# Kernel optimization log

Hardware: AMD Instinct MI355X
Metric: run time of the kernel (lower is better)

## Reference

```python
import jax, jax.numpy as jnp
import numpy as np

B, D, K, BETA = 32, 64, 1024, 0.25


def _conv(x, w, b, s=1, p=0):
    y = jax.lax.conv_general_dilated(x, w, (s, s), [(p, p), (p, p)],
                                     dimension_numbers=('NCHW', 'OIHW', 'NCHW'))
    return y + b[None, :, None, None]


def _tconv(x, w, b):
    # PyTorch ConvTranspose2d(k=4, s=2, p=1); w layout (C_in, C_out, 4, 4)
    wt = jnp.flip(w, (2, 3)).transpose(1, 0, 2, 3)
    y = jax.lax.conv_general_dilated(x, wt, (1, 1), [(2, 2), (2, 2)],
                                     lhs_dilation=(2, 2),
                                     dimension_numbers=('NCHW', 'OIHW', 'NCHW'))
    return y + b[None, :, None, None]


def _res(x, w1, b1, w2, b2):
    # Residual: x + conv1x1(relu(conv3x3(relu(x))))  (no BN config)
    h = _conv(jax.nn.relu(x), w1, b1, 1, 1)
    h = _conv(jax.nn.relu(h), w2, b2, 1, 0)
    return x + h


def setup_inputs() -> dict:
    ks = iter(jax.random.split(jax.random.key(0), 64))

    def w(*shape):
        fan = int(np.prod(shape[1:]))
        return (jax.random.normal(next(ks), shape, jnp.float32) / np.sqrt(fan)).astype(jnp.float32)

    def z(n):
        return jnp.zeros((n,), jnp.float32)

    inp = dict(
        x=jax.random.normal(next(ks), (B, 3, 256, 256), jnp.float32),
        enc_w0=w(64, 3, 4, 4), enc_b0=z(64),
        enc_w1=w(128, 64, 4, 4), enc_b1=z(128),
        enc_w2=w(256, 128, 4, 4), enc_b2=z(256),
        enc_r0_w1=w(64, 256, 3, 3), enc_r0_b1=z(64),
        enc_r0_w2=w(256, 64, 1, 1), enc_r0_b2=z(256),
        enc_r1_w1=w(64, 256, 3, 3), enc_r1_b1=z(64),
        enc_r1_w2=w(256, 64, 1, 1), enc_r1_b2=z(256),
        enc_adj_w=w(D, 256, 1, 1), enc_adj_b=z(D),
        codebook=(jax.random.normal(next(ks), (K, D), jnp.float32) / np.sqrt(D)).astype(jnp.float32),
        dec_adj_w=w(256, D, 1, 1), dec_adj_b=z(256),
        dec_r0_w1=w(64, 256, 3, 3), dec_r0_b1=z(64),
        dec_r0_w2=w(256, 64, 1, 1), dec_r0_b2=z(256),
        dec_r1_w1=w(64, 256, 3, 3), dec_r1_b1=z(64),
        dec_r1_w2=w(256, 64, 1, 1), dec_r1_b2=z(256),
        dec_tw0=w(256, 128, 4, 4), dec_tb0=z(128),
        dec_tw1=w(128, 64, 4, 4), dec_tb1=z(64),
        dec_tw2=w(64, 32, 4, 4), dec_tb2=z(32),
        out_w=w(3, 32, 1, 1), out_b=z(3),
    )
    return inp


def reference(x, enc_w0, enc_b0, enc_w1, enc_b1, enc_w2, enc_b2,
              enc_r0_w1, enc_r0_b1, enc_r0_w2, enc_r0_b2,
              enc_r1_w1, enc_r1_b1, enc_r1_w2, enc_r1_b2,
              enc_adj_w, enc_adj_b, codebook, dec_adj_w, dec_adj_b,
              dec_r0_w1, dec_r0_b1, dec_r0_w2, dec_r0_b2,
              dec_r1_w1, dec_r1_b1, dec_r1_w2, dec_r1_b2,
              dec_tw0, dec_tb0, dec_tw1, dec_tb1, dec_tw2, dec_tb2,
              out_w, out_b):
    # ---------- encoder (M=7: three stride-2 convs, no BN) ----------
    h = jax.nn.relu(_conv(x, enc_w0, enc_b0, 2, 1))   # [B,64,128,128]
    h = jax.nn.relu(_conv(h, enc_w1, enc_b1, 2, 1))   # [B,128,64,64]
    h = jax.nn.relu(_conv(h, enc_w2, enc_b2, 2, 1))   # [B,256,32,32]
    h = _res(h, enc_r0_w1, enc_r0_b1, enc_r0_w2, enc_r0_b2)
    h = _res(h, enc_r1_w1, enc_r1_b1, enc_r1_w2, enc_r1_b2)
    zlat = _conv(h, enc_adj_w, enc_adj_b)             # [B,D,32,32]
    # ---------- vector quantization ----------
    zp = zlat.transpose(0, 2, 3, 1)                   # [B,32,32,D]
    zf = zp.reshape(-1, D)                            # [N,D], N = B*32*32
    d = (jnp.sum(zf * zf, 1, keepdims=True)
         - 2.0 * (zf @ codebook.T)
         + jnp.sum(codebook * codebook, 1)[None, :])  # [N,K]
    idx = jnp.argmin(d, axis=1)                       # [N] codebook indices
    q = codebook[idx].reshape(zp.shape)
    sg = jax.lax.stop_gradient
    e_loss = jnp.mean((sg(q) - zp) ** 2)              # commitment
    q_loss = jnp.mean((q - sg(zp)) ** 2)              # codebook
    vq_loss = q_loss + BETA * e_loss
    q_st = zp + sg(q - zp)                            # straight-through
    counts = jnp.zeros((K,), jnp.float32).at[idx].add(1.0)
    probs = counts / zf.shape[0]
    perplexity = jnp.exp(-jnp.sum(probs * jnp.log(probs + 1e-10)))
    hq = q_st.transpose(0, 3, 1, 2)                   # [B,D,32,32]
    # ---------- decoder (M=7: three stride-2 transposed convs) ----------
    h = _conv(hq, dec_adj_w, dec_adj_b)               # [B,256,32,32]
    h = _res(h, dec_r0_w1, dec_r0_b1, dec_r0_w2, dec_r0_b2)
    h = _res(h, dec_r1_w1, dec_r1_b1, dec_r1_w2, dec_r1_b2)
    h = jax.nn.relu(_tconv(h, dec_tw0, dec_tb0))      # [B,128,64,64]
    h = jax.nn.relu(_tconv(h, dec_tw1, dec_tb1))      # [B,64,128,128]
    h = jax.nn.relu(_tconv(h, dec_tw2, dec_tb2))      # [B,32,256,256]
    x_recon = _conv(h, out_w, out_b)                  # [B,3,256,256]
    return x_recon, vq_loss, perplexity
```

## Files before the change

### kernel.cpp

```cpp
#include <hip/hip_runtime.h>
#include <math.h>

typedef __attribute__((ext_vector_type(4))) float f32x4;
typedef __attribute__((ext_vector_type(8))) short short8;
typedef __attribute__((ext_vector_type(4))) unsigned int u32x4;
typedef unsigned short ushort_t;
typedef unsigned int uint_t;

static const size_t A_OFF      = 0;
static const size_t C_OFF      = 0;
static const size_t D_OFF      = 9469952;
static const size_t E_OFF      = 18939904;
static const size_t Q_OFF      = 21037056;
static const size_t B_OFF      = 34611200;
static const size_t CBT_OFF    = 52453376;
static const size_t CNORM_OFF  = 52518912;
static const size_t COUNTS_OFF = 52519936;
static const size_t SUMSQ_OFF  = 52520960;
static const size_t WT_OFF     = 52520964;

__device__ __forceinline__ ushort_t f2b(float f) {
  uint_t u = __float_as_uint(f);
  uint_t r = (u + 0x7FFFu + ((u >> 16) & 1u)) >> 16;
  return (ushort_t)r;
}
__device__ __forceinline__ float b2f(ushort_t h) {
  return __uint_as_float(((uint_t)h) << 16);
}

__global__ void k_wt_conv(const float* __restrict__ w, float* __restrict__ wT,
                          int Cin, int Cout, int K) {
  const int n = Cin * Cout * K;
  for (int i = blockIdx.x * 256 + threadIdx.x; i < n; i += gridDim.x * 256) {
    const int co = i % Cout;
    const int k  = (i / Cout) % K;
    const int ci = i / (Cout * K);
    wT[i] = w[((size_t)co * Cin + ci) * K + k];
  }
}
__global__ void k_wtb(const float* __restrict__ w, ushort_t* __restrict__ wbT,
                      int Cin, int Cout) {
  const int n = 4 * Cout * Cin * 4;
  for (int i = blockIdx.x * 256 + threadIdx.x; i < n; i += gridDim.x * 256) {
    const int tap = i & 3;
    const int ci  = (i >> 2) % Cin;
    const int co  = ((i >> 2) / Cin) % Cout;
    const int ph  = (i >> 2) / (Cin * Cout);
    const int ey = ph >> 1, ex = ph & 1;
    const int ty = tap >> 1, tx = tap & 1;
    const int kidx = (3 - 2 * ty - ey) * 4 + (3 - 2 * tx - ex);
    wbT[i] = f2b(w[((size_t)ci * Cout + co) * 16 + kidx]);
  }
}
__global__ void k_wsplit(const float* __restrict__ w, ushort_t* __restrict__ wh,
                         ushort_t* __restrict__ wl, int n) {
  for (int i = blockIdx.x * 256 + threadIdx.x; i < n; i += gridDim.x * 256) {
    const float v = w[i];
    const ushort_t h = f2b(v);
    wh[i] = h;
    wl[i] = f2b(v - b2f(h));
  }
}
__global__ void k_wt3split(const float* __restrict__ w, ushort_t* __restrict__ wh,
                           ushort_t* __restrict__ wl) {
  const int n = 9 * 64 * 256;
  for (int i = blockIdx.x * 256 + threadIdx.x; i < n; i += gridDim.x * 256) {
    const int ci = i & 255;
    const int co = (i >> 8) & 63;
    const int t  = i >> 14;
    const float v = w[((size_t)co * 256 + ci) * 9 + t];
    const ushort_t h = f2b(v);
    wh[i] = h;
    wl[i] = f2b(v - b2f(h));
  }
}
__global__ void k_cbt(const float* __restrict__ cb, float* __restrict__ cbT,
                      float* __restrict__ cnorm) {
  const int c = blockIdx.x * 256 + threadIdx.x;
  float s = 0.0f;
  for (int ci = 0; ci < 64; ++ci) {
    const float v = cb[(size_t)c * 64 + ci];
    s += v * v;
    cbT[(size_t)ci * 1024 + c] = v;
  }
  cnorm[c] = s;
}

__global__ __launch_bounds__(256) void k_conv4s2_s3(
    const float* __restrict__ in, const float* __restrict__ wT,
    const float* __restrict__ bias, float* __restrict__ out) {
  const int b   = blockIdx.z;
  const int co0 = blockIdx.y << 4;
  const int oy0 = (blockIdx.x >> 2) << 5;
  const int ox0 = (blockIdx.x & 3) << 5;
  const int tid = threadIdx.x;
  const int ty = tid >> 4, tx = tid & 15;
  __shared__ float tin[3][66][67];
  float acc[4][16];
#pragma unroll
  for (int p = 0; p < 4; ++p)
#pragma unroll
    for (int co = 0; co < 16; ++co) acc[p][co] = 0.0f;

  const int iy0 = (oy0 << 1) - 1, ix0 = (ox0 << 1) - 1;
  for (int c = 0; c < 3; ++c) {
    const float* ip = in + (size_t)(b * 3 + c) * 65536;
    for (int j = tid; j < 66 * 66; j += 256) {
      const int r = j / 66, col = j - r * 66;
      const int iy = iy0 + r, ix = ix0 + col;
      float v = 0.0f;
      if ((unsigned)iy < 256u && (unsigned)ix < 256u) v = ip[iy * 256 + ix];
      tin[c][r][col] = v;
    }
  }
  __syncthreads();
#pragma unroll
  for (int c = 0; c < 3; ++c) {
    const float* wp = wT + (size_t)c * 16 * 64 + co0;
#pragma unroll
    for (int ky = 0; ky < 4; ++ky)
#pragma unroll
      for (int kx = 0; kx < 4; ++kx) {
        const float v0 = tin[c][2 * ty + ky][2 * tx + kx];
        const float v1 = tin[c][2 * ty + ky][2 * tx + 32 + kx];
        const float v2 = tin[c][2 * ty + 32 + ky][2 * tx + kx];
        const float v3 = tin[c][2 * ty + 32 + ky][2 * tx + 32 + kx];
        const float* wk = wp + (ky * 4 + kx) * 64;
#pragma unroll
        for (int co = 0; co < 16; ++co) {
          const float wv = wk[co];
          acc[0][co] = fmaf(v0, wv, acc[0][co]);
          acc[1][co] = fmaf(v1, wv, acc[1][co]);
          acc[2][co] = fmaf(v2, wv, acc[2][co]);
          acc[3][co] = fmaf(v3, wv, acc[3][co]);
        }
      }
  }
#pragma unroll
  for (int co = 0; co < 16; ++co) {
    const float bv = bias[co0 + co];
    float* op = out + (size_t)(b * 64 + co0 + co) * 16900;
    op[(size_t)(oy0 + ty + 1) * 130 + ox0 + tx + 1]        = fmaxf(acc[0][co] + bv, 0.0f);
    op[(size_t)(oy0 + ty + 1) * 130 + ox0 + tx + 17]       = fmaxf(acc[1][co] + bv, 0.0f);
    op[(size_t)(oy0 + ty + 17) * 130 + ox0 + tx + 1]       = fmaxf(acc[2][co] + bv, 0.0f);
    op[(size_t)(oy0 + ty + 17) * 130 + ox0 + tx + 17]      = fmaxf(acc[3][co] + bv, 0.0f);
  }
}

template <int WSHIFT, int CIN, int COUT, int WP, int INSTRIDE, int WOP, int OUTSTRIDE>
__global__ __launch_bounds__(256) void k_conv4s2_mfma(
    const float* __restrict__ in, const ushort_t* __restrict__ wbh,
    const ushort_t* __restrict__ wbl, const float* __restrict__ bias,
    float* __restrict__ out) {
  constexpr int W = 1 << WSHIFT;
  constexpr int NCH = CIN / 2;
  __shared__ __align__(16) short lsAh[64 * 40];
  __shared__ __align__(16) short lsAl[64 * 40];
  __shared__ __align__(16) short lsBh[64 * 40];
  __shared__ __align__(16) short lsBl[64 * 40];

  const int tid = threadIdx.x;
  const int b = blockIdx.z;
  const int co_b0 = blockIdx.y << 6;
  const int pxb0 = blockIdx.x << 6;

  const int spx = tid & 63;
  const int kg  = tid >> 6;
  const int sy = (pxb0 + spx) >> WSHIFT;
  const int sx = (pxb0 + spx) & (W - 1);
  const float* ipa = in + (size_t)(b * CIN + (kg >> 1)) * INSTRIDE
                   + (size_t)(2 * sy + 2 * (kg & 1)) * WP + 2 * sx;
  const ushort_t* wbase_h = wbh + (size_t)(co_b0 + spx) * (CIN * 16) + kg * 8;
  const ushort_t* wbase_l = wbl + (size_t)(co_b0 + spx) * (CIN * 16) + kg * 8;

  const int lane = tid & 63, wid = tid >> 6;
  const int wm = wid & 1, wn = wid >> 1;
  const int arow = lane & 15, ag = lane >> 4;

  f32x4 acc[2][2];
#pragma unroll
  for (int m = 0; m < 2; ++m)
#pragma unroll
    for (int n = 0; n < 2; ++n) acc[m][n] = (f32x4){0.f, 0.f, 0.f, 0.f};

  float pa[8];
  u32x4 pbh, pbl;
  auto loadch = [&](int ch) {
    const float* p = ipa + (size_t)ch * 2 * INSTRIDE;
    pa[0] = p[0];  pa[1] = p[1];      pa[2] = p[2];      pa[3] = p[3];
    pa[4] = p[WP]; pa[5] = p[WP + 1]; pa[6] = p[WP + 2]; pa[7] = p[WP + 3];
    pbh = *(const u32x4*)(wbase_h + (size_t)ch * 32);
    pbl = *(const u32x4*)(wbase_l + (size_t)ch * 32);
  };

  loadch(0);
  for (int ch = 0; ch < NCH; ++ch) {
    __syncthreads();
    u32x4 vh, vl;
#pragma unroll
    for (int j = 0; j < 4; ++j) {
      const ushort_t h0 = f2b(pa[2 * j]);
      const ushort_t h1 = f2b(pa[2 * j + 1]);
      const ushort_t l0 = f2b(pa[2 * j] - b2f(h0));
      const ushort_t l1 = f2b(pa[2 * j + 1] - b2f(h1));
      vh[j] = (uint_t)h0 | ((uint_t)h1 << 16);
      vl[j] = (uint_t)l0 | ((uint_t)l1 << 16);
    }
    *(u32x4*)(&lsAh[spx * 40 + kg * 8]) = vh;
    *(u32x4*)(&lsAl[spx * 40 + kg * 8]) = vl;
    *(u32x4*)(&lsBh[spx * 40 + kg * 8]) = pbh;
    *(u32x4*)(&lsBl[spx * 40 + kg * 8]) = pbl;
    if (ch + 1 < NCH) loadch(ch + 1);
    __syncthreads();
    short8 ah[2], al[2], bh[2], bl[2];
#pragma unroll
    for (int m = 0; m < 2; ++m) {
      ah[m] = *(const short8*)(&lsAh[(wm * 32 + m * 16 + arow) * 40 + ag * 8]);
      al[m] = *(const short8*)(&lsAl[(wm * 32 + m * 16 + arow) * 40 + ag * 8]);
    }
#pragma unroll
    for (int n = 0; n < 2; ++n) {
      bh[n] = *(const short8*)(&lsBh[(wn * 32 + n * 16 + arow) * 40 + ag * 8]);
      bl[n] = *(const short8*)(&lsBl[(wn * 32 + n * 16 + arow) * 40 + ag * 8]);
    }
#pragma unroll
    for (int m = 0; m < 2; ++m)
#pragma unroll
      for (int n = 0; n < 2; ++n) {
        acc[m][n] = __builtin_amdgcn_mfma_f32_16x16x32_bf16(ah[m], bh[n], acc[m][n], 0, 0, 0);
        acc[m][n] = __builtin_amdgcn_mfma_f32_16x16x32_bf16(ah[m], bl[n], acc[m][n], 0, 0, 0);
        acc[m][n] = __builtin_amdgcn_mfma_f32_16x16x32_bf16(al[m], bh[n], acc[m][n], 0, 0, 0);
      }
  }

#pragma unroll
  for (int m = 0; m < 2; ++m)
#pragma unroll
    for (int n = 0; n < 2; ++n) {
      const int col = co_b0 + wn * 32 + n * 16 + arow;
      const float bv = bias[col];
      float* obase = out + (size_t)(b * COUT + col) * OUTSTRIDE;
#pragma unroll
      for (int r = 0; r < 4; ++r) {
        const int pxl = pxb0 + wm * 32 + m * 16 + ag * 4 + r;
        const int yy = pxl >> WSHIFT, xx = pxl & (W - 1);
        obase[(size_t)(yy + 1) * WOP + (xx + 1)] = fmaxf(acc[m][n][r] + bv, 0.0f);
      }
    }
}

__global__ __launch_bounds__(512) void k_conv3x3_mfma(
    const float* __restrict__ in, const ushort_t* __restrict__ w3h,
    const ushort_t* __restrict__ w3l, const float* __restrict__ bias,
    float* __restrict__ out) {
  __shared__ __align__(16) short lsAh[64 * 40];
  __shared__ __align__(16) short lsAl[64 * 40];
  __shared__ __align__(16) short lsBh[64 * 40];
  __shared__ __align__(16) short lsBl[64 * 40];

  const int tid = threadIdx.x;
  const int b = blockIdx.z;
  const int pxb0 = blockIdx.x << 6;
  const bool isA = tid < 256;
  const int sidx = tid & 63;
  const int skg  = (tid >> 6) & 3;

  const int py = (pxb0 + sidx) >> 5;
  const int pxx = (pxb0 + sidx) & 31;
  const float* ipa = in + (size_t)b * 256 * 1156 + (size_t)(py)*34 + pxx;

  const int lane = tid & 63, wid = tid >> 6;
  const int wm = wid & 1, wn = wid >> 1;
  const int arow = lane & 15, ag = lane >> 4;

  f32x4 acc[2];
  acc[0] = (f32x4){0.f, 0.f, 0.f, 0.f};
  acc[1] = (f32x4){0.f, 0.f, 0.f, 0.f};

  float pa[8];
  u32x4 pbh, pbl;
  auto loadit = [&](int it) {
    const int t = it >> 3, ck = it & 7;
    if (isA) {
      const int dy = t / 3, dx = t - 3 * (t / 3);
      const float* p = ipa + (size_t)(ck * 32 + skg * 8) * 1156 + dy * 34 + dx;
#pragma unroll
      for (int j = 0; j < 8; ++j) pa[j] = p[(size_t)j * 1156];
    } else {
      const ushort_t* ph = w3h + ((size_t)(t * 64 + sidx) << 8) + ck * 32 + skg * 8;
      const ushort_t* pl = w3l + ((size_t)(t * 64 + sidx) << 8) + ck * 32 + skg * 8;
      pbh = *(const u32x4*)ph;
      pbl = *(const u32x4*)pl;
    }
  };

  loadit(0);
  for (int it = 0; it < 72; ++it) {
    __syncthreads();
    if (isA) {
      u32x4 vh, vl;
#pragma unroll
      for (int j = 0; j < 4; ++j) {
        const float v0 = fmaxf(pa[2 * j], 0.0f);
        const float v1 = fmaxf(pa[2 * j + 1], 0.0f);
        const ushort_t h0 = f2b(v0);
        const ushort_t h1 = f2b(v1);
        const ushort_t l0 = f2b(v0 - b2f(h0));
        const ushort_t l1 = f2b(v1 - b2f(h1));
        vh[j] = (uint_t)h0 | ((uint_t)h1 << 16);
        vl[j] = (uint_t)l0 | ((uint_t)l1 << 16);
      }
      *(u32x4*)(&lsAh[sidx * 40 + skg * 8]) = vh;
      *(u32x4*)(&lsAl[sidx * 40 + skg * 8]) = vl;
    } else {
      *(u32x4*)(&lsBh[sidx * 40 + skg * 8]) = pbh;
      *(u32x4*)(&lsBl[sidx * 40 + skg * 8]) = pbl;
    }
    if (it + 1 < 72) loadit(it + 1);
    __syncthreads();
    short8 ah[2], al[2];
#pragma unroll
    for (int m = 0; m < 2; ++m) {
      ah[m] = *(const short8*)(&lsAh[(wm * 32 + m * 16 + arow) * 40 + ag * 8]);
      al[m] = *(const short8*)(&lsAl[(wm * 32 + m * 16 + arow) * 40 + ag * 8]);
    }
    const short8 bh = *(const short8*)(&lsBh[(wn * 16 + arow) * 40 + ag * 8]);
    const short8 bl = *(const short8*)(&lsBl[(wn * 16 + arow) * 40 + ag * 8]);
#pragma unroll
    for (int m = 0; m < 2; ++m) {
      acc[m] = __builtin_amdgcn_mfma_f32_16x16x32_bf16(ah[m], bh, acc[m], 0, 0, 0);
      acc[m] = __builtin_amdgcn_mfma_f32_16x16x32_bf16(ah[m], bl, acc[m], 0, 0, 0);
      acc[m] = __builtin_amdgcn_mfma_f32_16x16x32_bf16(al[m], bh, acc[m], 0, 0, 0);
    }
  }

  const int col = wn * 16 + arow;
  const float bv = bias[col];
  float* obase = out + (size_t)(b * 64 + col) * 1024;
#pragma unroll
  for (int m = 0; m < 2; ++m)
#pragma unroll
    for (int r = 0; r < 4; ++r) {
      const int pxl = pxb0 + wm * 32 + m * 16 + ag * 4 + r;
      obase[pxl] = acc[m][r] + bv;
    }
}

template <int IN_RELU, int HAS_RES, int IN_PAD, int OUT_PAD>
__global__ __launch_bounds__(256) void k_conv1x1_px(
    const float* __restrict__ in, const float* __restrict__ wT,
    const float* __restrict__ bias, const float* __restrict__ res,
    float* __restrict__ out, int Cin, int Cout) {
  const int b   = blockIdx.z;
  const int co0 = blockIdx.y << 4;
  const int px  = blockIdx.x * 256 + threadIdx.x;
  const int ppad = 35 + px + 2 * (px >> 5);
  const int ioff = IN_PAD ? ppad : px;
  const int istr = IN_PAD ? 1156 : 1024;
  const int ooff = OUT_PAD ? ppad : px;
  const int ostr = OUT_PAD ? 1156 : 1024;
  float acc[16];
#pragma unroll
  for (int co = 0; co < 16; ++co) acc[co] = 0.0f;
  const float* ip = in + (size_t)b * Cin * istr + ioff;
  const float* wp = wT + co0;
  for (int ci = 0; ci < Cin; ++ci) {
    float v = *ip;
    if (IN_RELU) v = fmaxf(v, 0.0f);
    ip += istr;
#pragma unroll
    for (int co = 0; co < 16; ++co) acc[co] = fmaf(v, wp[co], acc[co]);
    wp += Cout;
  }
  float* op = out + (size_t)(b * Cout + co0) * ostr + ooff;
  const float* rp = res + (size_t)(b * Cout + co0) * ostr + ooff;
#pragma unroll
  for (int co = 0; co < 16; ++co) {
    float r = acc[co] + bias[co0 + co];
    if (HAS_RES) r += rp[(size_t)co * ostr];
    op[(size_t)co * ostr] = r;
  }
}

template <int PXB, int COB, int WSHIFT, int CIN, int COUT, int WP,
          int INSTRIDE, int WOP, int OUTSTRIDE, int FINAL, int GRP>
__global__ __launch_bounds__(256) void k_tconv_mfma(
    const float* __restrict__ in, const ushort_t* __restrict__ wbT,
    const float* __restrict__ bias, const float* __restrict__ ow,
    const float* __restrict__ ob, float* __restrict__ out) {
  constexpr int W = 1 << WSHIFT;
  constexpr int NCH = CIN / 8;
  constexpr int NGRP = NCH / GRP;
  constexpr int PXSH = (PXB == 64) ? 6 : 7;
  constexpr int COSH = (COB == 64) ? 6 : 5;
  constexpr int NKG = (PXB * 4) / 256;
  constexpr int KGSTEP = 256 / PXB;
  __shared__ __align__(16) short lsA[GRP][PXB * 40];
  __shared__ __align__(16) short lsB[GRP][COB * 40];
  __shared__ float pxco[FINAL ? PXB : 1][33];

  const int tid = threadIdx.x;
  const int b = blockIdx.z;
  const int phase = blockIdx.y & 3;
  const int ey = phase >> 1, ex = phase & 1;
  const int co_b0 = (blockIdx.y >> 2) * COB;
  const int pxb0 = blockIdx.x * PXB;

  const int spx = tid & (PXB - 1);
  const int kg0 = tid >> PXSH;
  const int sy = (pxb0 + spx) >> WSHIFT;
  const int sx = (pxb0 + spx) & (W - 1);
  const float* ipa = in + (size_t)b * CIN * INSTRIDE + (size_t)(sy + ey) * WP + (sx + ex);
  const int sco = tid & (COB - 1);
  const int skg = tid >> COSH;
  const bool bstage = (tid < COB * 4);
  const ushort_t* wrow = wbT + ((size_t)(phase * COUT + co_b0 + sco) * CIN) * 4;

  const int lane = tid & 63, wid = tid >> 6;
  const int wm = wid % (PXB / 32), wn = wid / (PXB / 32);
  const int arow = lane & 15, ag = lane >> 4;

  f32x4 acc[2][2];
#pragma unroll
  for (int m = 0; m < 2; ++m)
#pragma unroll
    for (int n = 0; n < 2; ++n) acc[m][n] = (f32x4){0.f, 0.f, 0.f, 0.f};

  float pa[GRP][NKG][8];
  u32x4 pb[GRP];
  auto loadgrp = [&](int g) {
#pragma unroll
    for (int c = 0; c < GRP; ++c) {
      const int ch = g * GRP + c;
#pragma unroll
      for (int k = 0; k < NKG; ++k) {
        const float* p = ipa + (size_t)(ch * 8 + (kg0 + k * KGSTEP) * 2) * INSTRIDE;
        const float* q = p + INSTRIDE;
        pa[c][k][0] = p[0]; pa[c][k][1] = p[1]; pa[c][k][2] = p[WP]; pa[c][k][3] = p[WP + 1];
        pa[c][k][4] = q[0]; pa[c][k][5] = q[1]; pa[c][k][6] = q[WP]; pa[c][k][7] = q[WP + 1];
      }
      if (bstage) pb[c] = *(const u32x4*)(wrow + (size_t)ch * 32 + skg * 8);
    }
  };

  loadgrp(0);
  for (int g = 0; g < NGRP; ++g) {
    __syncthreads();
#pragma unroll
    for (int c = 0; c < GRP; ++c) {
#pragma unroll
      for (int k = 0; k < NKG; ++k) {
        u32x4 pk;
        pk[0] = (uint_t)f2b(pa[c][k][0]) | ((uint_t)f2b(pa[c][k][1]) << 16);
        pk[1] = (uint_t)f2b(pa[c][k][2]) | ((uint_t)f2b(pa[c][k][3]) << 16);
        pk[2] = (uint_t)f2b(pa[c][k][4]) | ((uint_t)f2b(pa[c][k][5]) << 16);
        pk[3] = (uint_t)f2b(pa[c][k][6]) | ((uint_t)f2b(pa[c][k][7]) << 16);
        *(u32x4*)(&lsA[c][spx * 40 + (kg0 + k * KGSTEP) * 8]) = pk;
      }
      if (bstage) *(u32x4*)(&lsB[c][sco * 40 + skg * 8]) = pb[c];
    }
    if (g + 1 < NGRP) loadgrp(g + 1);
    __syncthreads();
#pragma unroll
    for (int c = 0; c < GRP; ++c) {
      const short8 a0 = *(const short8*)(&lsA[c][(wm * 32 + arow) * 40 + ag * 8]);
      const short8 a1 = *(const short8*)(&lsA[c][(wm * 32 + 16 + arow) * 40 + ag * 8]);
      const short8 b0 = *(const short8*)(&lsB[c][(wn * 32 + arow) * 40 + ag * 8]);
      const short8 b1 = *(const short8*)(&lsB[c][(wn * 32 + 16 + arow) * 40 + ag * 8]);
      acc[0][0] = __builtin_amdgcn_mfma_f32_16x16x32_bf16(a0, b0, acc[0][0], 0, 0, 0);
      acc[0][1] = __builtin_amdgcn_mfma_f32_16x16x32_bf16(a0, b1, acc[0][1], 0, 0, 0);
      acc[1][0] = __builtin_amdgcn_mfma_f32_16x16x32_bf16(a1, b0, acc[1][0], 0, 0, 0);
      acc[1][1] = __builtin_amdgcn_mfma_f32_16x16x32_bf16(a1, b1, acc[1][1], 0, 0, 0);
    }
  }

  if constexpr (!FINAL) {
#pragma unroll
    for (int m = 0; m < 2; ++m)
#pragma unroll
      for (int n = 0; n < 2; ++n) {
        const int col = co_b0 + wn * 32 + n * 16 + arow;
        const float bv = bias[col];
        float* obase = out + (size_t)(b * COUT + col) * OUTSTRIDE;
#pragma unroll
        for (int r = 0; r < 4; ++r) {
          const int pxl = pxb0 + wm * 32 + m * 16 + ag * 4 + r;
          const int yy = pxl >> WSHIFT, xx = pxl & (W - 1);
          obase[(size_t)(2 * yy + ey + 1) * WOP + (2 * xx + ex + 1)] =
              fmaxf(acc[m][n][r] + bv, 0.0f);
        }
      }
  } else {
#pragma unroll
    for (int m = 0; m < 2; ++m)
#pragma unroll
      for (int n = 0; n < 2; ++n) {
        const int col = wn * 32 + n * 16 + arow;
        const float bv = bias[col];
#pragma unroll
        for (int r = 0; r < 4; ++r) {
          const int pxl = wm * 32 + m * 16 + ag * 4 + r;
          pxco[pxl][col] = fmaxf(acc[m][n][r] + bv, 0.0f);
        }
      }
    __syncthreads();
    if (tid < PXB) {
      const int pxg = pxb0 + tid;
      const int yy = pxg >> WSHIFT, xx = pxg & (W - 1);
      const int oy = 2 * yy + ey, ox = 2 * xx + ex;
      float o0 = ob[0], o1 = ob[1], o2 = ob[2];
#pragma unroll
      for (int co = 0; co < 32; ++co) {
        const float v = pxco[tid][co];
        o0 = fmaf(ow[co], v, o0);
        o1 = fmaf(ow[32 + co], v, o1);
        o2 = fmaf(ow[64 + co], v, o2);
      }
      out[((size_t)(b * 3 + 0) * 256 + oy) * 256 + ox] = o0;
      out[((size_t)(b * 3 + 1) * 256 + oy) * 256 + ox] = o1;
      out[((size_t)(b * 3 + 2) * 256 + oy) * 256 + ox] = o2;
    }
  }
}

__global__ __launch_bounds__(256) void k_vq(
    const float* __restrict__ zlat, const float* __restrict__ cbT,
    const float* __restrict__ cnorm, const float* __restrict__ cb,
    float* __restrict__ q, float* __restrict__ counts, float* __restrict__ sumsq) {
  const int tid = threadIdx.x;
  const int px0 = blockIdx.x << 4;
  const int b   = px0 >> 10;
  const int pl0 = px0 & 1023;
  __shared__ float zT[64][17];
  __shared__ float rd[16][256];
  __shared__ int   ri[16][256];
  for (int j = tid; j < 1024; j += 256) {
    const int ci = j >> 4, p = j & 15;
    zT[ci][p] = zlat[(size_t)(b * 64 + ci) * 1024 + pl0 + p];
  }
  __syncthreads();
  float dot[4][16];
#pragma unroll
  for (int k = 0; k < 4; ++k)
#pragma unroll
    for (int p = 0; p < 16; ++p) dot[k][p] = 0.0f;
  for (int ci = 0; ci < 64; ++ci) {
    float z[16];
#pragma unroll
    for (int p = 0; p < 16; ++p) z[p] = zT[ci][p];
#pragma unroll
    for (int k = 0; k < 4; ++k) {
      const float cv = cbT[(size_t)ci * 1024 + (k << 8) + tid];
#pragma unroll
      for (int p = 0; p < 16; ++p) dot[k][p] = fmaf(cv, z[p], dot[k][p]);
    }
  }
  float bd[16]; int bi[16];
#pragma unroll
  for (int p = 0; p < 16; ++p) { bd[p] = 3.4e38f; bi[p] = 0; }
#pragma unroll
  for (int k = 0; k < 4; ++k) {
    const int c = (k << 8) + tid;
    const float cn = cnorm[c];
#pragma unroll
    for (int p = 0; p < 16; ++p) {
      const float d = cn - 2.0f * dot[k][p];
      if (d < bd[p]) { bd[p] = d; bi[p] = c; }
    }
  }
#pragma unroll
  for (int p = 0; p < 16; ++p) { rd[p][tid] = bd[p]; ri[p][tid] = bi[p]; }
  __syncthreads();
  for (int s = 128; s >= 1; s >>= 1) {
    if (tid < s) {
#pragma unroll
      for (int p = 0; p < 16; ++p) {
        const float d2 = rd[p][tid + s]; const int i2 = ri[p][tid + s];
        const float d1 = rd[p][tid];     const int i1 = ri[p][tid];
        if (d2 < d1 || (d2 == d1 && i2 < i1)) { rd[p][tid] = d2; ri[p][tid] = i2; }
      }
    }
    __syncthreads();
  }
  if (tid < 16) atomicAdd(&counts[ri[tid][0]], 1.0f);
  const int p    = tid >> 4;
  const int best = ri[p][0];
  const int cb0  = (tid & 15) << 2;
  float ss = 0.0f;
  float* qp = q + (size_t)b * 65536 + pl0 + p;
#pragma unroll
  for (int cc = 0; cc < 4; ++cc) {
    const int ci = cb0 + cc;
    const float qv = cb[(size_t)best * 64 + ci];
    const float zv = zT[ci][p];
    const float df = qv - zv;
    ss += df * df;
    qp[(size_t)ci * 1024] = qv;
  }
#pragma unroll
  for (int o = 32; o > 0; o >>= 1) ss += __shfl_down(ss, o);
  if ((tid & 63) == 0) atomicAdd(sumsq, ss);
}

__global__ void k_final(const float* __restrict__ counts, const float* __restrict__ sumsq,
                        float* __restrict__ out2) {
  const int tid = threadIdx.x;
  float h = 0.0f;
  for (int k = tid; k < 1024; k += 256) {
    const float pr = counts[k] * (1.0f / 32768.0f);
    h -= pr * logf(pr + 1e-10f);
  }
#pragma unroll
  for (int o = 32; o > 0; o >>= 1) h += __shfl_down(h, o);
  __shared__ float hs[4];
  if ((tid & 63) == 0) hs[tid >> 6] = h;
  __syncthreads();
  if (tid == 0) {
    out2[0] = 1.25f * sumsq[0] * (1.0f / 2097152.0f);
    out2[1] = expf(hs[0] + hs[1] + hs[2] + hs[3]);
  }
}

extern "C" void kernel_launch(void* const* d_in, const int* in_sizes, int n_in,
                              void* d_out, int out_size, void* d_ws, size_t ws_size,
                              hipStream_t stream) {
  const float* x        = (const float*)d_in[0];
  const float* enc_w0   = (const float*)d_in[1];
  const float* enc_b0   = (const float*)d_in[2];
  const float* enc_w1   = (const float*)d_in[3];
  const float* enc_b1   = (const float*)d_in[4];
  const float* enc_w2   = (const float*)d_in[5];
  const float* enc_b2   = (const float*)d_in[6];
  const float* er0w1    = (const float*)d_in[7];
  const float* er0b1    = (const float*)d_in[8];
  const float* er0w2    = (const float*)d_in[9];
  const float* er0b2    = (const float*)d_in[10];
  const float* er1w1    = (const float*)d_in[11];
  const float* er1b1    = (const float*)d_in[12];
  const float* er1w2    = (const float*)d_in[13];
  const float* er1b2    = (const float*)d_in[14];
  const float* eadj_w   = (const float*)d_in[15];
  const float* eadj_b   = (const float*)d_in[16];
  const float* codebook = (const float*)d_in[17];
  const float* dadj_w   = (const float*)d_in[18];
  const float* dadj_b   = (const float*)d_in[19];
  const float* dr0w1    = (const float*)d_in[20];
  const float* dr0b1    = (const float*)d_in[21];
  const float* dr0w2    = (const float*)d_in[22];
  const float* dr0b2    = (const float*)d_in[23];
  const float* dr1w1    = (const float*)d_in[24];
  const float* dr1b1    = (const float*)d_in[25];
  const float* dr1w2    = (const float*)d_in[26];
  const float* dr1b2    = (const float*)d_in[27];
  const float* tw0      = (const float*)d_in[28];
  const float* tb0      = (const float*)d_in[29];
  const float* tw1      = (const float*)d_in[30];
  const float* tb1      = (const float*)d_in[31];
  const float* tw2      = (const float*)d_in[32];
  const float* tb2      = (const float*)d_in[33];
  const float* out_w    = (const float*)d_in[34];
  const float* out_b    = (const float*)d_in[35];

  float* ws = (float*)d_ws;
  float* A      = ws + A_OFF;
  float* Bb     = ws + B_OFF;
  float* C      = ws + C_OFF;
  float* Dq     = ws + D_OFF;
  float* E      = ws + E_OFF;
  float* Q      = ws + Q_OFF;
  float* cbT    = ws + CBT_OFF;
  float* cnorm  = ws + CNORM_OFF;
  float* counts = ws + COUNTS_OFF;
  float* sumsq  = ws + SUMSQ_OFF;

  size_t o = WT_OFF;
  float* wt_enc0  = ws + o; o += (size_t)3 * 16 * 64;
  float* wt_er0w2 = ws + o; o += (size_t)64 * 256;
  float* wt_er1w2 = ws + o; o += (size_t)64 * 256;
  float* wt_eadj  = ws + o; o += (size_t)256 * 64;
  float* wt_dadj  = ws + o; o += (size_t)64 * 256;
  float* wt_dr0w2 = ws + o; o += (size_t)64 * 256;
  float* wt_dr1w2 = ws + o; o += (size_t)64 * 256;
  ushort_t* wbT0 = (ushort_t*)(ws + o); o += 262144;
  ushort_t* wbT1 = (ushort_t*)(ws + o); o += 65536;
  ushort_t* wbT2 = (ushort_t*)(ws + o); o += 16384;
  ushort_t* wsh1 = (ushort_t*)(ws + o); o += 65536;
  ushort_t* wsl1 = (ushort_t*)(ws + o); o += 65536;
  ushort_t* wsh2 = (ushort_t*)(ws + o); o += 262144;
  ushort_t* wsl2 = (ushort_t*)(ws + o); o += 262144;
  ushort_t* w3h_er0 = (ushort_t*)(ws + o); o += 73728;
  ushort_t* w3l_er0 = (ushort_t*)(ws + o); o += 73728;
  ushort_t* w3h_er1 = (ushort_t*)(ws + o); o += 73728;
  ushort_t* w3l_er1 = (ushort_t*)(ws + o); o += 73728;
  ushort_t* w3h_dr0 = (ushort_t*)(ws + o); o += 73728;
  ushort_t* w3l_dr0 = (ushort_t*)(ws + o); o += 73728;
  ushort_t* w3h_dr1 = (ushort_t*)(ws + o); o += 73728;
  ushort_t* w3l_dr1 = (ushort_t*)(ws + o); o += 73728;

  float* fout = (float*)d_out;

  #define GB(n) (((n) + 255) / 256)
  hipMemsetAsync(ws, 0, WT_OFF * sizeof(float), stream);

  k_wt_conv<<<GB(3 * 64 * 16), 256, 0, stream>>>(enc_w0, wt_enc0, 3, 64, 16);
  k_wt_conv<<<GB(64 * 256), 256, 0, stream>>>(er0w2, wt_er0w2, 64, 256, 1);
  k_wt_conv<<<GB(64 * 256), 256, 0, stream>>>(er1w2, wt_er1w2, 64, 256, 1);
  k_wt_conv<<<GB(256 * 64), 256, 0, stream>>>(eadj_w, wt_eadj, 256, 64, 1);
  k_wt_conv<<<GB(64 * 256), 256, 0, stream>>>(dadj_w, wt_dadj, 64, 256, 1);
  k_wt_conv<<<GB(64 * 256), 256, 0, stream>>>(dr0w2, wt_dr0w2, 64, 256, 1);
  k_wt_conv<<<GB(64 * 256), 256, 0, stream>>>(dr1w2, wt_dr1w2, 64, 256, 1);
  k_wtb<<<GB(524288), 256, 0, stream>>>(tw0, wbT0, 256, 128);
  k_wtb<<<GB(131072), 256, 0, stream>>>(tw1, wbT1, 128, 64);
  k_wtb<<<GB(32768), 256, 0, stream>>>(tw2, wbT2, 64, 32);
  k_wsplit<<<GB(131072), 256, 0, stream>>>(enc_w1, wsh1, wsl1, 131072);
  k_wsplit<<<GB(524288), 256, 0, stream>>>(enc_w2, wsh2, wsl2, 524288);
  k_wt3split<<<GB(147456), 256, 0, stream>>>(er0w1, w3h_er0, w3l_er0);
  k_wt3split<<<GB(147456), 256, 0, stream>>>(er1w1, w3h_er1, w3l_er1);
  k_wt3split<<<GB(147456), 256, 0, stream>>>(dr0w1, w3h_dr0, w3l_dr0);
  k_wt3split<<<GB(147456), 256, 0, stream>>>(dr1w1, w3h_dr1, w3l_dr1);
  k_cbt<<<4, 256, 0, stream>>>(codebook, cbT, cnorm);

  k_conv4s2_s3<<<dim3(16, 4, 32), 256, 0, stream>>>(x, wt_enc0, enc_b0, A);
  k_conv4s2_mfma<6, 64, 128, 130, 16900, 66, 4356>
      <<<dim3(64, 2, 32), 256, 0, stream>>>(A, wsh1, wsl1, enc_b1, Bb);
  hipMemsetAsync(ws, 0, (size_t)18939904 * sizeof(float), stream);
  k_conv4s2_mfma<5, 128, 256, 66, 4356, 34, 1156>
      <<<dim3(16, 4, 32), 256, 0, stream>>>(Bb, wsh2, wsl2, enc_b2, C);
  k_conv3x3_mfma<<<dim3(16, 1, 32), 512, 0, stream>>>(C, w3h_er0, w3l_er0, er0b1, E);
  k_conv1x1_px<1, 1, 0, 1><<<dim3(4, 16, 32), 256, 0, stream>>>(E, wt_er0w2, er0b2, C, Dq, 64, 256);
  k_conv3x3_mfma<<<dim3(16, 1, 32), 512, 0, stream>>>(Dq, w3h_er1, w3l_er1, er1b1, E);
  k_conv1x1_px<1, 1, 0, 1><<<dim3(4, 16, 32), 256, 0, stream>>>(E, wt_er1w2, er1b2, Dq, C, 64, 256);
  k_conv1x1_px<0, 0, 1, 0><<<dim3(4, 4, 32), 256, 0, stream>>>(C, wt_eadj, eadj_b, nullptr, E, 256, 64);
  k_vq<<<2048, 256, 0, stream>>>(E, cbT, cnorm, codebook, Q, counts, sumsq);
  k_conv1x1_px<0, 0, 0, 1><<<dim3(4, 16, 32), 256, 0, stream>>>(Q, wt_dadj, dadj_b, nullptr, C, 64, 256);
  k_conv3x3_mfma<<<dim3(16, 1, 32), 512, 0, stream>>>(C, w3h_dr0, w3l_dr0, dr0b1, E);
  k_conv1x1_px<1, 1, 0, 1><<<dim3(4, 16, 32), 256, 0, stream>>>(E, wt_dr0w2, dr0b2, C, Dq, 64, 256);
  k_conv3x3_mfma<<<dim3(16, 1, 32), 512, 0, stream>>>(Dq, w3h_dr1, w3l_dr1, dr1b1, E);
  k_conv1x1_px<1, 1, 0, 1><<<dim3(4, 16, 32), 256, 0, stream>>>(E, wt_dr1w2, dr1b2, Dq, C, 64, 256);
  k_tconv_mfma<64, 64, 5, 256, 128, 34, 1156, 66, 4356, 0, 2>
      <<<dim3(16, 8, 32), 256, 0, stream>>>(C, wbT0, tb0, nullptr, nullptr, Bb);
  hipMemsetAsync(ws, 0, (size_t)34611200 * sizeof(float), stream);
  k_tconv_mfma<64, 64, 6, 128, 64, 66, 4356, 130, 16900, 0, 2>
      <<<dim3(64, 4, 32), 256, 0, stream>>>(Bb, wbT1, tb1, nullptr, nullptr, A);
  k_tconv_mfma<128, 32, 7, 64, 32, 130, 16900, 0, 0, 1, 1>
      <<<dim3(128, 4, 32), 256, 0, stream>>>(A, wbT2, tb2, out_w, out_b, fout);
  k_final<<<1, 256, 0, stream>>>(counts, sumsq, fout + 6291456);
  #undef GB
}
```

Baseline: 1.764 ms.

## Fuse residual conv3x3 and conv1x1 into one MFMA kernel; zero only halos

Each residual block's 3x3 conv and its following 1x1 conv, residual add and ReLU are merged into one MFMA kernel. The 64-channel intermediate stays in LDS as a bf16 hi/lo split, and the 1x1 weights are pre-split to bf16 pairs. Large hipMemsetAsync calls over the workspace are replaced by small kernels that zero only the padding ring of each padded plane, plus the VQ counters. This removes the intermediate global round trip and several hundred MB of memset traffic. In exchange the fused kernel reads 1x1 weights straight from global memory and does extra split-bf16 MFMAs, which may change accuracy slightly.

```diff
diff --git a/kernel.cpp b/kernel.cpp
--- a/kernel.cpp
+++ b/kernel.cpp
@@ -26,6 +26,28 @@
 }
 __device__ __forceinline__ float b2f(ushort_t h) {
   return __uint_as_float(((uint_t)h) << 16);
+}
+
+__global__ void k_halo(float* __restrict__ buf, int HP, int WP) {
+  const int plane = blockIdx.x;
+  float* p = buf + (size_t)plane * HP * WP;
+  const int ring = 2 * (HP + WP) - 4;
+  for (int i = threadIdx.x; i < ring; i += blockDim.x) {
+    int idx;
+    if (i < WP) idx = i;
+    else if (i < 2 * WP) idx = (HP - 1) * WP + (i - WP);
+    else {
+      const int j = i - 2 * WP;
+      const int r = 1 + (j >> 1);
+      idx = r * WP + ((j & 1) ? (WP - 1) : 0);
+    }
+    p[idx] = 0.0f;
+  }
+}
+__global__ void k_zero(float* __restrict__ counts, float* __restrict__ sumsq) {
+  const int t = blockIdx.x * 256 + threadIdx.x;
+  if (t < 1024) counts[t] = 0.0f;
+  if (t == 0) sumsq[0] = 0.0f;
 }
 
 __global__ void k_wt_conv(const float* __restrict__ w, float* __restrict__ wT,
@@ -249,14 +271,16 @@
     }
 }
 
-__global__ __launch_bounds__(512) void k_conv3x3_mfma(
+__global__ __launch_bounds__(512) void k_res_mfma(
     const float* __restrict__ in, const ushort_t* __restrict__ w3h,
-    const ushort_t* __restrict__ w3l, const float* __restrict__ bias,
-    float* __restrict__ out) {
-  __shared__ __align__(16) short lsAh[64 * 40];
-  __shared__ __align__(16) short lsAl[64 * 40];
-  __shared__ __align__(16) short lsBh[64 * 40];
-  __shared__ __align__(16) short lsBl[64 * 40];
+    const ushort_t* __restrict__ w3l, const float* __restrict__ b1,
+    const ushort_t* __restrict__ w2h, const ushort_t* __restrict__ w2l,
+    const float* __restrict__ b2, float* __restrict__ out) {
+  __shared__ __align__(16) short smem[10240];
+  short* lsAh = smem;
+  short* lsAl = smem + 2560;
+  short* lsBh = smem + 5120;
+  short* lsBl = smem + 7680;
 
   const int tid = threadIdx.x;
   const int b = blockIdx.z;
@@ -267,7 +291,7 @@
 
   const int py = (pxb0 + sidx) >> 5;
   const int pxx = (pxb0 + sidx) & 31;
-  const float* ipa = in + (size_t)b * 256 * 1156 + (size_t)(py)*34 + pxx;
+  const float* ipa = in + (size_t)b * 256 * 1156 + (size_t)py * 34 + pxx;
 
   const int lane = tid & 63, wid = tid >> 6;
   const int wm = wid & 1, wn = wid >> 1;
@@ -334,16 +358,57 @@
     }
   }
 
-  const int col = wn * 16 + arow;
-  const float bv = bias[col];
-  float* obase = out + (size_t)(b * 64 + col) * 1024;
-#pragma unroll
-  for (int m = 0; m < 2; ++m)
+  __syncthreads();
+  {
+    const float bv = b1[wn * 16 + arow];
+    short* hh = smem;
+    short* hl = smem + 4608;
+#pragma unroll
+    for (int m = 0; m < 2; ++m)
+#pragma unroll
+      for (int r = 0; r < 4; ++r) {
+        const int pxl = wm * 32 + m * 16 + ag * 4 + r;
+        const float v = fmaxf(acc[m][r] + bv, 0.0f);
+        const ushort_t h = f2b(v);
+        hh[pxl * 72 + wn * 16 + arow] = (short)h;
+        hl[pxl * 72 + wn * 16 + arow] = (short)f2b(v - b2f(h));
+      }
+  }
+  __syncthreads();
+
+  const int m2 = wid & 3;
+  const int nh = wid >> 2;
+  const short* hh = smem;
+  const short* hl = smem + 4608;
+  short8 a2h[2], a2l[2];
+#pragma unroll
+  for (int c = 0; c < 2; ++c) {
+    a2h[c] = *(const short8*)(&hh[(m2 * 16 + arow) * 72 + c * 32 + ag * 8]);
+    a2l[c] = *(const short8*)(&hl[(m2 * 16 + arow) * 72 + c * 32 + ag * 8]);
+  }
+#pragma unroll
+  for (int j = 0; j < 8; ++j) {
+    const int col2 = (nh * 8 + j) * 16 + arow;
+    f32x4 acc2 = (f32x4){0.f, 0.f, 0.f, 0.f};
+#pragma unroll
+    for (int c = 0; c < 2; ++c) {
+      const short8 b2h_ = *(const short8*)(w2h + (size_t)col2 * 64 + c * 32 + ag * 8);
+      const short8 b2l_ = *(const short8*)(w2l + (size_t)col2 * 64 + c * 32 + ag * 8);
+      acc2 = __builtin_amdgcn_mfma_f32_16x16x32_bf16(a2h[c], b2h_, acc2, 0, 0, 0);
+      acc2 = __builtin_amdgcn_mfma_f32_16x16x32_bf16(a2h[c], b2l_, acc2, 0, 0, 0);
+      acc2 = __builtin_amdgcn_mfma_f32_16x16x32_bf16(a2l[c], b2h_, acc2, 0, 0, 0);
+    }
+    const float bv2 = b2[col2];
+    float* obase = out + (size_t)(b * 256 + col2) * 1156;
+    const float* rbase = in + (size_t)(b * 256 + col2) * 1156;
 #pragma unroll
     for (int r = 0; r < 4; ++r) {
-      const int pxl = pxb0 + wm * 32 + m * 16 + ag * 4 + r;
-      obase[pxl] = acc[m][r] + bv;
-    }
+      const int px = pxb0 + m2 * 16 + ag * 4 + r;
+      const int yy = px >> 5, xx = px & 31;
+      const int idx = (yy + 1) * 34 + xx + 1;
+      obase[idx] = acc2[r] + bv2 + rbase[idx];
+    }
+  }
 }
 
 template <int IN_RELU, int HAS_RES, int IN_PAD, int OUT_PAD>
@@ -675,12 +740,8 @@
 
   size_t o = WT_OFF;
   float* wt_enc0  = ws + o; o += (size_t)3 * 16 * 64;
-  float* wt_er0w2 = ws + o; o += (size_t)64 * 256;
-  float* wt_er1w2 = ws + o; o += (size_t)64 * 256;
   float* wt_eadj  = ws + o; o += (size_t)256 * 64;
   float* wt_dadj  = ws + o; o += (size_t)64 * 256;
-  float* wt_dr0w2 = ws + o; o += (size_t)64 * 256;
-  float* wt_dr1w2 = ws + o; o += (size_t)64 * 256;
   ushort_t* wbT0 = (ushort_t*)(ws + o); o += 262144;
   ushort_t* wbT1 = (ushort_t*)(ws + o); o += 65536;
   ushort_t* wbT2 = (ushort_t*)(ws + o); o += 16384;
@@ -696,19 +757,25 @@
   ushort_t* w3l_dr0 = (ushort_t*)(ws + o); o += 73728;
   ushort_t* w3h_dr1 = (ushort_t*)(ws + o); o += 73728;
   ushort_t* w3l_dr1 = (ushort_t*)(ws + o); o += 73728;
+  ushort_t* w2h_er0 = (ushort_t*)(ws + o); o += 8192;
+  ushort_t* w2l_er0 = (ushort_t*)(ws + o); o += 8192;
+  ushort_t* w2h_er1 = (ushort_t*)(ws + o); o += 8192;
+  ushort_t* w2l_er1 = (ushort_t*)(ws + o); o += 8192;
+  ushort_t* w2h_dr0 = (ushort_t*)(ws + o); o += 8192;
+  ushort_t* w2l_dr0 = (ushort_t*)(ws + o); o += 8192;
+  ushort_t* w2h_dr1 = (ushort_t*)(ws + o); o += 8192;
+  ushort_t* w2l_dr1 = (ushort_t*)(ws + o); o += 8192;
 
   float* fout = (float*)d_out;
 
   #define GB(n) (((n) + 255) / 256)
-  hipMemsetAsync(ws, 0, WT_OFF * sizeof(float), stream);
+  k_zero<<<4, 256, 0, stream>>>(counts, sumsq);
+  k_halo<<<2048, 64, 0, stream>>>(A, 130, 130);
+  k_halo<<<4096, 64, 0, stream>>>(Bb, 66, 66);
 
   k_wt_conv<<<GB(3 * 64 * 16), 256, 0, stream>>>(enc_w0, wt_enc0, 3, 64, 16);
-  k_wt_conv<<<GB(64 * 256), 256, 0, stream>>>(er0w2, wt_er0w2, 64, 256, 1);
-  k_wt_conv<<<GB(64 * 256), 256, 0, stream>>>(er1w2, wt_er1w2, 64, 256, 1);
   k_wt_conv<<<GB(256 * 64), 256, 0, stream>>>(eadj_w, wt_eadj, 256, 64, 1);
   k_wt_conv<<<GB(64 * 256), 256, 0, stream>>>(dadj_w, wt_dadj, 64, 256, 1);
-  k_wt_conv<<<GB(64 * 256), 256, 0, stream>>>(dr0w2, wt_dr0w2, 64, 256, 1);
-  k_wt_conv<<<GB(64 * 256), 256, 0, stream>>>(dr1w2, wt_dr1w2, 64, 256, 1);
   k_wtb<<<GB(524288), 256, 0, stream>>>(tw0, wbT0, 256, 128);
   k_wtb<<<GB(131072), 256, 0, stream>>>(tw1, wbT1, 128, 64);
   k_wtb<<<GB(32768), 256, 0, stream>>>(tw2, wbT2, 64, 32);
@@ -718,28 +785,33 @@
   k_wt3split<<<GB(147456), 256, 0, stream>>>(er1w1, w3h_er1, w3l_er1);
   k_wt3split<<<GB(147456), 256, 0, stream>>>(dr0w1, w3h_dr0, w3l_dr0);
   k_wt3split<<<GB(147456), 256, 0, stream>>>(dr1w1, w3h_dr1, w3l_dr1);
+  k_wsplit<<<GB(16384), 256, 0, stream>>>(er0w2, w2h_er0, w2l_er0, 16384);
+  k_wsplit<<<GB(16384), 256, 0, stream>>>(er1w2, w2h_er1, w2l_er1, 16384);
+  k_wsplit<<<GB(16384), 256, 0, stream>>>(dr0w2, w2h_dr0, w2l_dr0, 16384);
+  k_wsplit<<<GB(16384), 256, 0, stream>>>(dr1w2, w2h_dr1, w2l_dr1, 16384);
   k_cbt<<<4, 256, 0, stream>>>(codebook, cbT, cnorm);
 
   k_conv4s2_s3<<<dim3(16, 4, 32), 256, 0, stream>>>(x, wt_enc0, enc_b0, A);
   k_conv4s2_mfma<6, 64, 128, 130, 16900, 66, 4356>
       <<<dim3(64, 2, 32), 256, 0, stream>>>(A, wsh1, wsl1, enc_b1, Bb);
-  hipMemsetAsync(ws, 0, (size_t)18939904 * sizeof(float), stream);
+  k_halo<<<8192, 64, 0, stream>>>(C, 34, 34);
+  k_halo<<<8192, 64, 0, stream>>>(Dq, 34, 34);
   k_conv4s2_mfma<5, 128, 256, 66, 4356, 34, 1156>
       <<<dim3(16, 4, 32), 256, 0, stream>>>(Bb, wsh2, wsl2, enc_b2, C);
-  k_conv3x3_mfma<<<dim3(16, 1, 32), 512, 0, stream>>>(C, w3h_er0, w3l_er0, er0b1, E);
-  k_conv1x1_px<1, 1, 0, 1><<<dim3(4, 16, 32), 256, 0, stream>>>(E, wt_er0w2, er0b2, C, Dq, 64, 256);
-  k_conv3x3_mfma<<<dim3(16, 1, 32), 512, 0, stream>>>(Dq, w3h_er1, w3l_er1, er1b1, E);
-  k_conv1x1_px<1, 1, 0, 1><<<dim3(4, 16, 32), 256, 0, stream>>>(E, wt_er1w2, er1b2, Dq, C, 64, 256);
+  k_res_mfma<<<dim3(16, 1, 32), 512, 0, stream>>>(C, w3h_er0, w3l_er0, er0b1,
+                                                  w2h_er0, w2l_er0, er0b2, Dq);
+  k_res_mfma<<<dim3(16, 1, 32), 512, 0, stream>>>(Dq, w3h_er1, w3l_er1, er1b1,
+                                                  w2h_er1, w2l_er1, er1b2, C);
   k_conv1x1_px<0, 0, 1, 0><<<dim3(4, 4, 32), 256, 0, stream>>>(C, wt_eadj, eadj_b, nullptr, E, 256, 64);
   k_vq<<<2048, 256, 0, stream>>>(E, cbT, cnorm, codebook, Q, counts, sumsq);
   k_conv1x1_px<0, 0, 0, 1><<<dim3(4, 16, 32), 256, 0, stream>>>(Q, wt_dadj, dadj_b, nullptr, C, 64, 256);
-  k_conv3x3_mfma<<<dim3(16, 1, 32), 512, 0, stream>>>(C, w3h_dr0, w3l_dr0, dr0b1, E);
-  k_conv1x1_px<1, 1, 0, 1><<<dim3(4, 16, 32), 256, 0, stream>>>(E, wt_dr0w2, dr0b2, C, Dq, 64, 256);
-  k_conv3x3_mfma<<<dim3(16, 1, 32), 512, 0, stream>>>(Dq, w3h_dr1, w3l_dr1, dr1b1, E);
-  k_conv1x1_px<1, 1, 0, 1><<<dim3(4, 16, 32), 256, 0, stream>>>(E, wt_dr1w2, dr1b2, Dq, C, 64, 256);
+  k_res_mfma<<<dim3(16, 1, 32), 512, 0, stream>>>(C, w3h_dr0, w3l_dr0, dr0b1,
+                                                  w2h_dr0, w2l_dr0, dr0b2, Dq);
+  k_res_mfma<<<dim3(16, 1, 32), 512, 0, stream>>>(Dq, w3h_dr1, w3l_dr1, dr1b1,
+                                                  w2h_dr1, w2l_dr1, dr1b2, C);
   k_tconv_mfma<64, 64, 5, 256, 128, 34, 1156, 66, 4356, 0, 2>
       <<<dim3(16, 8, 32), 256, 0, stream>>>(C, wbT0, tb0, nullptr, nullptr, Bb);
-  hipMemsetAsync(ws, 0, (size_t)34611200 * sizeof(float), stream);
+  k_halo<<<2048, 64, 0, stream>>>(A, 130, 130);
   k_tconv_mfma<64, 64, 6, 128, 64, 66, 4356, 130, 16900, 0, 2>
       <<<dim3(64, 4, 32), 256, 0, stream>>>(Bb, wbT1, tb1, nullptr, nullptr, A);
   k_tconv_mfma<128, 32, 7, 64, 32, 130, 16900, 0, 0, 1, 1>
```

New measurement: 1.773 ms. No clear change (+0.5%).
